# Kernel optimization log

Measured on AMD Instinct MI355X. Metric: run time of the kernel, lower is better.

Reference implementation:

```python
import jax, jax.numpy as jnp
import numpy as np

B, E, S = 32, 1024, 1024


def setup_inputs() -> dict:
    key = jax.random.key(0)
    k_x, k_w = jax.random.split(key)
    x = jax.random.normal(k_x, (B, E, S), dtype=jnp.float32)
    weight = jax.random.normal(k_w, (1, S), dtype=jnp.float32)
    bias = jnp.zeros((S,), dtype=jnp.float32)
    return {"x": x, "weight": weight, "bias": bias}


def _toeplitz(v):
    # v: (m,) -> M[i, j] = v[j - i] if j >= i else 0  (upper-triangular Toeplitz)
    m = v.shape[0]
    i = jnp.arange(m)[:, None]
    j = jnp.arange(m)[None, :]
    return jnp.where(j >= i, v[(j - i) % m], jnp.zeros((), dtype=v.dtype))


def reference(x, weight, bias):
    b, e, s = x.shape
    W = _toeplitz(weight.reshape(-1))          # (S, S)
    out = x.reshape(b * e, s) @ W + bias       # (B*E, S)
    return out.reshape(b, e, s)
```

## Files before the change

kernel.cpp:

```cpp
#include <hip/hip_runtime.h>
#include <stdint.h>

typedef __bf16 bf16x8 __attribute__((ext_vector_type(8)));
typedef float  f32x4  __attribute__((ext_vector_type(4)));

static constexpr int S_DIM = 1024;

__device__ __forceinline__ ushort f32_to_bf16_rne(float f) {
    uint32_t u = __builtin_bit_cast(uint32_t, f);
    u += 0x7fffu + ((u >> 16) & 1u);
    return (ushort)(u >> 16);
}
__device__ __forceinline__ uint32_t pk_bf16(float a, float b) {
    return (uint32_t)f32_to_bf16_rne(a) | ((uint32_t)f32_to_bf16_rne(b) << 16);
}

__global__ void build_wc(const float* __restrict__ w, ushort* __restrict__ Wc) {
    int c  = blockIdx.x * 256 + threadIdx.x;
    int kq = c >> 10;
    int j  = c & 1023;
    uint32_t p[4];
#pragma unroll
    for (int h = 0; h < 4; ++h) {
        int d0 = j - (kq * 8 + h * 2);
        int d1 = d0 - 1;
        float v0 = (d0 >= 0) ? w[d0] : 0.0f;
        float v1 = (d1 >= 0) ? w[d1] : 0.0f;
        p[h] = (uint32_t)f32_to_bf16_rne(v0) | ((uint32_t)f32_to_bf16_rne(v1) << 16);
    }
    reinterpret_cast<uint4*>(Wc)[c] = make_uint4(p[0], p[1], p[2], p[3]);
}

__global__ __launch_bounds__(256, 2) void toep_rowpanel(
    const float* __restrict__ x, const ushort* __restrict__ Wc,
    const float* __restrict__ bias, float* __restrict__ out)
{
    __shared__ __align__(16) ushort As[2][1024];

    const int tid  = threadIdx.x;
    const int lane = tid & 63;
    const int w    = tid >> 6;
    const int l15  = lane & 15;
    const int quad = lane >> 4;
    const int m0   = blockIdx.x * 32;

    const int sm = tid >> 3;
    const int kc = tid & 7;
    const float* gx = x + (size_t)(m0 + sm) * S_DIM + kc * 4;
    const int aw = (kc >> 1) * 256 + sm * 8 + (kc & 1) * 4;

    const ushort* gb = Wc + (size_t)quad * 8192 + w * 128 + l15 * 8;

    const int ar0 = quad * 256 + l15 * 8;
    const int ar1 = ar0 + 128;

    f32x4 acc[16][2] = {};

    f32x4 av0 = __builtin_nontemporal_load(reinterpret_cast<const f32x4*>(gx));
    f32x4 av1 = __builtin_nontemporal_load(reinterpret_cast<const f32x4*>(gx + 32));

    for (int it = 0; it < 32; ++it) {
        const int p = it & 1;
        int itn = it + 2; if (itn > 31) itn = 31;
        f32x4 avn = __builtin_nontemporal_load(reinterpret_cast<const f32x4*>(gx + itn * 32));

        uint32_t c0 = pk_bf16(av0[0], av0[1]);
        uint32_t c1 = pk_bf16(av0[2], av0[3]);
        *reinterpret_cast<uint2*>(&As[p][aw]) = make_uint2(c0, c1);

        const int t2   = it * 2;
        const int f_lo = (t2 > w) ? ((t2 - w + 3) >> 2) : 0;
        const bool g0 = f_lo < 4, g1 = f_lo < 8, g2 = f_lo < 12, g3 = f_lo < 16;

        const ushort* gbit = gb + (size_t)it * 32768;
        bf16x8 bf[4][4];
        if (g0) {
#pragma unroll
            for (int i = 0; i < 4; ++i)
                bf[0][i] = *reinterpret_cast<const bf16x8*>(gbit + 0 * 2048 + i * 512);
        }
        if (g1) {
#pragma unroll
            for (int i = 0; i < 4; ++i)
                bf[1][i] = *reinterpret_cast<const bf16x8*>(gbit + 1 * 2048 + i * 512);
        }
        if (g2) {
#pragma unroll
            for (int i = 0; i < 4; ++i)
                bf[2][i] = *reinterpret_cast<const bf16x8*>(gbit + 2 * 2048 + i * 512);
        }
        if (g3) {
#pragma unroll
            for (int i = 0; i < 4; ++i)
                bf[3][i] = *reinterpret_cast<const bf16x8*>(gbit + 3 * 2048 + i * 512);
        }

        asm volatile("s_waitcnt lgkmcnt(0)" ::: "memory");
        __builtin_amdgcn_s_barrier();
        asm volatile("" ::: "memory");

        bf16x8 af0 = *reinterpret_cast<const bf16x8*>(&As[p][ar0]);
        bf16x8 af1 = *reinterpret_cast<const bf16x8*>(&As[p][ar1]);

        if (g0) {
#pragma unroll
            for (int i = 0; i < 4; ++i) {
                acc[0 + i][0] = __builtin_amdgcn_mfma_f32_16x16x32_bf16(af0, bf[0][i], acc[0 + i][0], 0, 0, 0);
                acc[0 + i][1] = __builtin_amdgcn_mfma_f32_16x16x32_bf16(af1, bf[0][i], acc[0 + i][1], 0, 0, 0);
            }
        }
        if (g1) {
#pragma unroll
            for (int i = 0; i < 4; ++i) {
                acc[4 + i][0] = __builtin_amdgcn_mfma_f32_16x16x32_bf16(af0, bf[1][i], acc[4 + i][0], 0, 0, 0);
                acc[4 + i][1] = __builtin_amdgcn_mfma_f32_16x16x32_bf16(af1, bf[1][i], acc[4 + i][1], 0, 0, 0);
            }
        }
        if (g2) {
#pragma unroll
            for (int i = 0; i < 4; ++i) {
                acc[8 + i][0] = __builtin_amdgcn_mfma_f32_16x16x32_bf16(af0, bf[2][i], acc[8 + i][0], 0, 0, 0);
                acc[8 + i][1] = __builtin_amdgcn_mfma_f32_16x16x32_bf16(af1, bf[2][i], acc[8 + i][1], 0, 0, 0);
            }
        }
        if (g3) {
#pragma unroll
            for (int i = 0; i < 4; ++i) {
                acc[12 + i][0] = __builtin_amdgcn_mfma_f32_16x16x32_bf16(af0, bf[3][i], acc[12 + i][0], 0, 0, 0);
                acc[12 + i][1] = __builtin_amdgcn_mfma_f32_16x16x32_bf16(af1, bf[3][i], acc[12 + i][1], 0, 0, 0);
            }
        }

        av0 = av1; av1 = avn;
    }

#pragma unroll
    for (int f = 0; f < 16; ++f) {
        const int col = (f * 4 + w) * 16 + l15;
        const float bv = bias[col];
#pragma unroll
        for (int im = 0; im < 2; ++im) {
            const int row0 = m0 + im * 16 + quad * 4;
            float* op = out + (size_t)row0 * S_DIM + col;
#pragma unroll
            for (int r = 0; r < 4; ++r)
                __builtin_nontemporal_store(acc[f][im][r] + bv, op + (size_t)r * S_DIM);
        }
    }
}

extern "C" void kernel_launch(void* const* d_in, const int* in_sizes, int n_in,
                              void* d_out, int out_size, void* d_ws, size_t ws_size,
                              hipStream_t stream) {
    const float* x      = (const float*)d_in[0];
    const float* weight = (const float*)d_in[1];
    const float* bias   = (const float*)d_in[2];
    float* out          = (float*)d_out;

    ushort* Wc = (ushort*)d_ws;

    build_wc<<<512, 256, 0, stream>>>(weight, Wc);
    toep_rowpanel<<<1024, 256, 0, stream>>>(x, Wc, bias, out);
}
```

Before: 299.3 us.

## Widen row panel to 64 rows with 512-thread blocks and 2x32 column tiles

Each block now covers 64 rows with 8 waves instead of 32 rows with 4. Each wave owns two adjacent 16-column tiles per 256-column panel and reuses them across four 16-row A fragments, so each B fragment load from the Toeplitz weight feeds more MFMAs. The causal skip check is redone at the new tile granularity, and the x prefetch load is moved after the B loads. More rows per block means fewer B reloads overall, at the cost of larger blocks and possibly lower occupancy from the same register budget under 512-thread launch bounds.

```diff
diff --git a/kernel.cpp b/kernel.cpp
--- a/kernel.cpp
+++ b/kernel.cpp
@@ -31,120 +31,121 @@
     reinterpret_cast<uint4*>(Wc)[c] = make_uint4(p[0], p[1], p[2], p[3]);
 }
 
-__global__ __launch_bounds__(256, 2) void toep_rowpanel(
+__global__ __launch_bounds__(512, 2) void toep_rowpanel64(
     const float* __restrict__ x, const ushort* __restrict__ Wc,
     const float* __restrict__ bias, float* __restrict__ out)
 {
-    __shared__ __align__(16) ushort As[2][1024];
+    __shared__ __align__(16) ushort As[2][2048];
 
     const int tid  = threadIdx.x;
     const int lane = tid & 63;
     const int w    = tid >> 6;
     const int l15  = lane & 15;
     const int quad = lane >> 4;
-    const int m0   = blockIdx.x * 32;
+    const int m0   = blockIdx.x * 64;
 
     const int sm = tid >> 3;
     const int kc = tid & 7;
     const float* gx = x + (size_t)(m0 + sm) * S_DIM + kc * 4;
-    const int aw = (kc >> 1) * 256 + sm * 8 + (kc & 1) * 4;
+    const int aw = (kc >> 1) * 512 + sm * 8 + (kc & 1) * 4;
 
-    const ushort* gb = Wc + (size_t)quad * 8192 + w * 128 + l15 * 8;
+    const ushort* gb = Wc + (size_t)quad * 8192 + w * 256 + l15 * 8;
 
-    const int ar0 = quad * 256 + l15 * 8;
-    const int ar1 = ar0 + 128;
+    const int ar0 = quad * 512 + l15 * 8;
 
-    f32x4 acc[16][2] = {};
+    f32x4 acc[4][2][4] = {};
 
     f32x4 av0 = __builtin_nontemporal_load(reinterpret_cast<const f32x4*>(gx));
     f32x4 av1 = __builtin_nontemporal_load(reinterpret_cast<const f32x4*>(gx + 32));
 
     for (int it = 0; it < 32; ++it) {
         const int p = it & 1;
-        int itn = it + 2; if (itn > 31) itn = 31;
-        f32x4 avn = __builtin_nontemporal_load(reinterpret_cast<const f32x4*>(gx + itn * 32));
 
         uint32_t c0 = pk_bf16(av0[0], av0[1]);
         uint32_t c1 = pk_bf16(av0[2], av0[3]);
         *reinterpret_cast<uint2*>(&As[p][aw]) = make_uint2(c0, c1);
 
-        const int t2   = it * 2;
-        const int f_lo = (t2 > w) ? ((t2 - w + 3) >> 2) : 0;
-        const bool g0 = f_lo < 4, g1 = f_lo < 8, g2 = f_lo < 12, g3 = f_lo < 16;
+        bool g[4];
+#pragma unroll
+        for (int pi = 0; pi < 4; ++pi) g[pi] = (pi * 8 + w) >= it;
 
         const ushort* gbit = gb + (size_t)it * 32768;
-        bf16x8 bf[4][4];
-        if (g0) {
-#pragma unroll
-            for (int i = 0; i < 4; ++i)
-                bf[0][i] = *reinterpret_cast<const bf16x8*>(gbit + 0 * 2048 + i * 512);
+        bf16x8 bf[4][2];
+        if (g[0]) {
+            bf[0][0] = *reinterpret_cast<const bf16x8*>(gbit + 0 * 2048);
+            bf[0][1] = *reinterpret_cast<const bf16x8*>(gbit + 0 * 2048 + 128);
         }
-        if (g1) {
-#pragma unroll
-            for (int i = 0; i < 4; ++i)
-                bf[1][i] = *reinterpret_cast<const bf16x8*>(gbit + 1 * 2048 + i * 512);
+        if (g[1]) {
+            bf[1][0] = *reinterpret_cast<const bf16x8*>(gbit + 1 * 2048);
+            bf[1][1] = *reinterpret_cast<const bf16x8*>(gbit + 1 * 2048 + 128);
         }
-        if (g2) {
-#pragma unroll
-            for (int i = 0; i < 4; ++i)
-                bf[2][i] = *reinterpret_cast<const bf16x8*>(gbit + 2 * 2048 + i * 512);
+        if (g[2]) {
+            bf[2][0] = *reinterpret_cast<const bf16x8*>(gbit + 2 * 2048);
+            bf[2][1] = *reinterpret_cast<const bf16x8*>(gbit + 2 * 2048 + 128);
         }
-        if (g3) {
-#pragma unroll
-            for (int i = 0; i < 4; ++i)
-                bf[3][i] = *reinterpret_cast<const bf16x8*>(gbit + 3 * 2048 + i * 512);
+        if (g[3]) {
+            bf[3][0] = *reinterpret_cast<const bf16x8*>(gbit + 3 * 2048);
+            bf[3][1] = *reinterpret_cast<const bf16x8*>(gbit + 3 * 2048 + 128);
         }
+
+        int itn = it + 2; if (itn > 31) itn = 31;
+        f32x4 avn = __builtin_nontemporal_load(reinterpret_cast<const f32x4*>(gx + itn * 32));
 
         asm volatile("s_waitcnt lgkmcnt(0)" ::: "memory");
         __builtin_amdgcn_s_barrier();
         asm volatile("" ::: "memory");
 
-        bf16x8 af0 = *reinterpret_cast<const bf16x8*>(&As[p][ar0]);
-        bf16x8 af1 = *reinterpret_cast<const bf16x8*>(&As[p][ar1]);
+        bf16x8 af[4];
+#pragma unroll
+        for (int im = 0; im < 4; ++im)
+            af[im] = *reinterpret_cast<const bf16x8*>(&As[p][ar0 + im * 128]);
 
-        if (g0) {
+        if (g[0]) {
 #pragma unroll
-            for (int i = 0; i < 4; ++i) {
-                acc[0 + i][0] = __builtin_amdgcn_mfma_f32_16x16x32_bf16(af0, bf[0][i], acc[0 + i][0], 0, 0, 0);
-                acc[0 + i][1] = __builtin_amdgcn_mfma_f32_16x16x32_bf16(af1, bf[0][i], acc[0 + i][1], 0, 0, 0);
-            }
+            for (int h = 0; h < 2; ++h)
+#pragma unroll
+                for (int im = 0; im < 4; ++im)
+                    acc[0][h][im] = __builtin_amdgcn_mfma_f32_16x16x32_bf16(af[im], bf[0][h], acc[0][h][im], 0, 0, 0);
         }
-        if (g1) {
+        if (g[1]) {
 #pragma unroll
-            for (int i = 0; i < 4; ++i) {
-                acc[4 + i][0] = __builtin_amdgcn_mfma_f32_16x16x32_bf16(af0, bf[1][i], acc[4 + i][0], 0, 0, 0);
-                acc[4 + i][1] = __builtin_amdgcn_mfma_f32_16x16x32_bf16(af1, bf[1][i], acc[4 + i][1], 0, 0, 0);
-            }
+            for (int h = 0; h < 2; ++h)
+#pragma unroll
+                for (int im = 0; im < 4; ++im)
+                    acc[1][h][im] = __builtin_amdgcn_mfma_f32_16x16x32_bf16(af[im], bf[1][h], acc[1][h][im], 0, 0, 0);
         }
-        if (g2) {
+        if (g[2]) {
 #pragma unroll
-            for (int i = 0; i < 4; ++i) {
-                acc[8 + i][0] = __builtin_amdgcn_mfma_f32_16x16x32_bf16(af0, bf[2][i], acc[8 + i][0], 0, 0, 0);
-                acc[8 + i][1] = __builtin_amdgcn_mfma_f32_16x16x32_bf16(af1, bf[2][i], acc[8 + i][1], 0, 0, 0);
-            }
+            for (int h = 0; h < 2; ++h)
+#pragma unroll
+                for (int im = 0; im < 4; ++im)
+                    acc[2][h][im] = __builtin_amdgcn_mfma_f32_16x16x32_bf16(af[im], bf[2][h], acc[2][h][im], 0, 0, 0);
         }
-        if (g3) {
+        if (g[3]) {
 #pragma unroll
-            for (int i = 0; i < 4; ++i) {
-                acc[12 + i][0] = __builtin_amdgcn_mfma_f32_16x16x32_bf16(af0, bf[3][i], acc[12 + i][0], 0, 0, 0);
-                acc[12 + i][1] = __builtin_amdgcn_mfma_f32_16x16x32_bf16(af1, bf[3][i], acc[12 + i][1], 0, 0, 0);
-            }
+            for (int h = 0; h < 2; ++h)
+#pragma unroll
+                for (int im = 0; im < 4; ++im)
+                    acc[3][h][im] = __builtin_amdgcn_mfma_f32_16x16x32_bf16(af[im], bf[3][h], acc[3][h][im], 0, 0, 0);
         }
 
         av0 = av1; av1 = avn;
     }
 
 #pragma unroll
-    for (int f = 0; f < 16; ++f) {
-        const int col = (f * 4 + w) * 16 + l15;
-        const float bv = bias[col];
+    for (int pi = 0; pi < 4; ++pi) {
+        const int colb = pi * 256 + w * 32 + l15;
+        const float bv0 = bias[colb];
+        const float bv1 = bias[colb + 16];
 #pragma unroll
-        for (int im = 0; im < 2; ++im) {
+        for (int im = 0; im < 4; ++im) {
             const int row0 = m0 + im * 16 + quad * 4;
-            float* op = out + (size_t)row0 * S_DIM + col;
+            float* op = out + (size_t)row0 * S_DIM + colb;
 #pragma unroll
-            for (int r = 0; r < 4; ++r)
-                __builtin_nontemporal_store(acc[f][im][r] + bv, op + (size_t)r * S_DIM);
+            for (int r = 0; r < 4; ++r) {
+                __builtin_nontemporal_store(acc[pi][0][im][r] + bv0, op + (size_t)r * S_DIM);
+                __builtin_nontemporal_store(acc[pi][1][im][r] + bv1, op + (size_t)r * S_DIM + 16);
+            }
         }
     }
 }
@@ -160,5 +161,5 @@
     ushort* Wc = (ushort*)d_ws;
 
     build_wc<<<512, 256, 0, stream>>>(weight, Wc);
-    toep_rowpanel<<<1024, 256, 0, stream>>>(x, Wc, bias, out);
+    toep_rowpanel64<<<512, 512, 0, stream>>>(x, Wc, bias, out);
 }
```

Result: faster. 271.6 us (-9.2%).
